# Kernel tuning notes

Measured on AMD Instinct MI355X. Metric: run time of the kernel, lower is better.

The kernel has to match this reference:

```python
import jax, jax.numpy as jnp
import numpy as np

N_NODES = 100000
N_EDGES = 1600000
F_IN = 64
HEADS = 4
F_OUT = 16
NEG_SLOPE = 0.2


def setup_inputs() -> dict:
    key = jax.random.key(0)
    k1, k2, k3, k4, k5 = jax.random.split(key, 5)
    x = jax.random.normal(k1, (N_NODES, F_IN), dtype=jnp.float32)
    edge_index = jax.random.randint(k2, (2, N_EDGES), 0, N_NODES, dtype=jnp.int64)
    # Glorot-ish scaled params
    W = jax.random.normal(k3, (HEADS, F_IN, F_OUT), dtype=jnp.float32) / np.sqrt(F_IN)
    a_src = jax.random.normal(k4, (HEADS, F_OUT), dtype=jnp.float32) / np.sqrt(F_OUT)
    a_dst = jax.random.normal(k5, (HEADS, F_OUT), dtype=jnp.float32) / np.sqrt(F_OUT)
    bias = jnp.zeros((HEADS * F_OUT,), dtype=jnp.float32)
    return {"x": x, "edge_index": edge_index, "W": W, "a_src": a_src,
            "a_dst": a_dst, "bias": bias}


def reference(x, edge_index, W, a_src, a_dst, bias):
    """Graph-attention conv (GAT-style) over a point-cloud graph.

    x: [N, F_in] node features; edge_index: [2, E] (src, dst);
    W: [H, F_in, F_out]; a_src/a_dst: [H, F_out]; bias: [H*F_out].
    Returns [N, H*F_out].
    """
    N = x.shape[0]
    src, dst = edge_index[0], edge_index[1]

    # Per-head linear projection: [N, H, F_out]
    h = jnp.einsum('nf,hfo->nho', x, W)

    # Per-node attention logits (decomposed GAT form): [N, H]
    logit_s = jnp.einsum('nho,ho->nh', h, a_src)
    logit_d = jnp.einsum('nho,ho->nh', h, a_dst)

    # Per-edge raw attention: [E, H]
    e = jax.nn.leaky_relu(logit_s[src] + logit_d[dst], negative_slope=NEG_SLOPE)

    # Segment softmax over incoming edges of each dst node
    m = jax.ops.segment_max(e, dst, num_segments=N)        # [N, H]
    m = jax.lax.stop_gradient(m)                           # softmax shift invariance
    e_exp = jnp.exp(e - m[dst])                            # [E, H]
    denom = jax.ops.segment_sum(e_exp, dst, num_segments=N)  # [N, H]
    alpha = e_exp / (denom[dst] + 1e-16)                   # [E, H]

    # Weighted message aggregation: scatter-add to dst
    msg = h[src] * alpha[:, :, None]                       # [E, H, F_out]
    out = jax.ops.segment_sum(msg, dst, num_segments=N)    # [N, H, F_out]

    return out.reshape(N, -1) + bias
```

## Files before the change

### kernel.cpp

```cpp
#include <hip/hip_runtime.h>

constexpr int N_NODES_C = 100000;
constexpr int N_EDGES_C = 1600000;
constexpr int F_IN_C = 64;
constexpr int HEADS_C = 4;
constexpr int F_OUT_C = 16;
constexpr float NEG_SLOPE_C = 0.2f;

constexpr int BUCK_SHIFT = 8;
constexpr int BUCK_NODES = 1 << BUCK_SHIFT;
constexpr int NBUCK = (N_NODES_C + BUCK_NODES - 1) / BUCK_NODES;
constexpr int BUCK_CAP = 5120;
constexpr int PART_BLOCKS = 256;
constexpr int EDGES_PER_PART_BLOCK = (N_EDGES_C + PART_BLOCKS - 1) / PART_BLOCKS;

typedef __attribute__((ext_vector_type(8))) short short8v;
typedef __attribute__((ext_vector_type(4))) float f32x4;

static __device__ __forceinline__ unsigned short f2bf(float f)
{
    const unsigned u = __float_as_uint(f);
    return (unsigned short)((u + 0x7FFF + ((u >> 16) & 1)) >> 16);
}
static __device__ __forceinline__ float bf2f(unsigned short b)
{
    return __uint_as_float(((unsigned)b) << 16);
}

__global__ __launch_bounds__(256) void k_prep(
    const float* __restrict__ W, int* __restrict__ bucket_cursor,
    unsigned short* __restrict__ Bpack)
{
    const int t = threadIdx.x;
    for (int i = t; i < NBUCK; i += 256) bucket_cursor[i] = 0;
    for (int idx = t; idx < 4096; idx += 256) {
        const int j    = idx & 7;
        const int lane = (idx >> 3) & 63;
        const int nt   = (idx >> 9) & 3;
        const int kc   = (idx >> 11) & 1;
        const int col  = nt * 16 + (lane & 15);
        const int k    = kc * 32 + (lane >> 4) * 8 + j;
        Bpack[idx] = f2bf(W[(col >> 4) * 1024 + k * 16 + (col & 15)]);
    }
}

__global__ __launch_bounds__(256) void k_project(
    const float* __restrict__ x, const unsigned short* __restrict__ Bpack,
    const float* __restrict__ a_src, const float* __restrict__ a_dst,
    unsigned short* __restrict__ h, float* __restrict__ ls, float* __restrict__ ld)
{
    const int wid  = threadIdx.x >> 6;
    const int lane = threadIdx.x & 63;
    const int node0 = (blockIdx.x * 4 + wid) * 16;
    const int colg = lane & 15;
    const int kg   = lane >> 4;

    const int rowc = min(node0 + colg, N_NODES_C - 1);
    short8v afrag[2];
    #pragma unroll
    for (int kc = 0; kc < 2; ++kc) {
        const float4* xp = (const float4*)&x[(size_t)rowc * 64 + kc * 32 + kg * 8];
        const float4 q0 = xp[0];
        const float4 q1 = xp[1];
        afrag[kc][0] = (short)f2bf(q0.x); afrag[kc][1] = (short)f2bf(q0.y);
        afrag[kc][2] = (short)f2bf(q0.z); afrag[kc][3] = (short)f2bf(q0.w);
        afrag[kc][4] = (short)f2bf(q1.x); afrag[kc][5] = (short)f2bf(q1.y);
        afrag[kc][6] = (short)f2bf(q1.z); afrag[kc][7] = (short)f2bf(q1.w);
    }

    f32x4 acc[4] = {{0.f,0.f,0.f,0.f},{0.f,0.f,0.f,0.f},
                    {0.f,0.f,0.f,0.f},{0.f,0.f,0.f,0.f}};
    #pragma unroll
    for (int kc = 0; kc < 2; ++kc) {
        #pragma unroll
        for (int nt = 0; nt < 4; ++nt) {
            const short8v bfrag = *(const short8v*)&Bpack[((kc * 4 + nt) * 64 + lane) * 8];
            acc[nt] = __builtin_amdgcn_mfma_f32_16x16x32_bf16(afrag[kc], bfrag, acc[nt], 0, 0, 0);
        }
    }

    #pragma unroll
    for (int nt = 0; nt < 4; ++nt) {
        const float as_v = a_src[nt * 16 + colg];
        const float ad_v = a_dst[nt * 16 + colg];
        #pragma unroll
        for (int i = 0; i < 4; ++i) {
            const int node = node0 + kg * 4 + i;
            const float hv = acc[nt][i];
            float vs = hv * as_v;
            float vd = hv * ad_v;
            #pragma unroll
            for (int o = 8; o >= 1; o >>= 1) {
                vs += __shfl_xor(vs, o, 64);
                vd += __shfl_xor(vd, o, 64);
            }
            if (node < N_NODES_C) {
                h[(size_t)node * 64 + nt * 16 + colg] = f2bf(hv);
                if (colg == 0) {
                    ls[node * HEADS_C + nt] = vs;
                    ld[node * HEADS_C + nt] = vd;
                }
            }
        }
    }
}

__global__ __launch_bounds__(1024) void k_partition(
    const int* __restrict__ src, const int* __restrict__ dst,
    int* __restrict__ bucket_cursor, int* __restrict__ bucketed)
{
    __shared__ int cnt[NBUCK];
    __shared__ int base[NBUCK];
    const int t = threadIdx.x;
    for (int i = t; i < NBUCK; i += 1024) cnt[i] = 0;
    __syncthreads();
    const int e0 = blockIdx.x * EDGES_PER_PART_BLOCK;
    const int e1 = min(e0 + EDGES_PER_PART_BLOCK, N_EDGES_C);
    for (int e = e0 + t; e < e1; e += 1024)
        atomicAdd(&cnt[dst[e] >> BUCK_SHIFT], 1);
    __syncthreads();
    for (int i = t; i < NBUCK; i += 1024) {
        base[i] = atomicAdd(&bucket_cursor[i], cnt[i]);
        cnt[i] = 0;
    }
    __syncthreads();
    for (int e = e0 + t; e < e1; e += 1024) {
        const int d = dst[e];
        const int b = d >> BUCK_SHIFT;
        const int r = atomicAdd(&cnt[b], 1);
        const int p = base[b] + r;
        if (p < BUCK_CAP)
            bucketed[b * BUCK_CAP + p] = src[e] | ((d & (BUCK_NODES - 1)) << 17);
    }
}

__global__ __launch_bounds__(256) void k_buildcsr(
    const int* __restrict__ bucket_cursor, const int* __restrict__ bucketed,
    int* __restrict__ csr_src, int* __restrict__ off, int* __restrict__ deg)
{
    __shared__ int hist[BUCK_NODES];
    __shared__ int pfx[BUCK_NODES];
    __shared__ int stageIn[BUCK_CAP];
    __shared__ int stageOut[BUCK_CAP];
    const int b = blockIdx.x;
    const int t = threadIdx.x;
    const int node0 = b * BUCK_NODES;
    const int nNodes = min(BUCK_NODES, N_NODES_C - node0);
    const int cnt = min(bucket_cursor[b], BUCK_CAP);
    const int* eb = &bucketed[(size_t)b * BUCK_CAP];

    hist[t] = 0;
    __syncthreads();
    for (int e = t; e < cnt; e += 256) {
        const int v = eb[e];
        stageIn[e] = v;
        atomicAdd(&hist[v >> 17], 1);
    }
    __syncthreads();
    const int myDeg = hist[t];
    pfx[t] = myDeg;
    __syncthreads();
    #pragma unroll
    for (int o = 1; o < BUCK_NODES; o <<= 1) {
        const int v = (t >= o) ? pfx[t - o] : 0;
        __syncthreads();
        pfx[t] += v;
        __syncthreads();
    }
    const int excl = pfx[t] - myDeg;
    if (t < nNodes) {
        deg[node0 + t] = myDeg;
        off[node0 + t] = b * BUCK_CAP + excl;
    }
    pfx[t] = excl;
    __syncthreads();
    for (int e = t; e < cnt; e += 256) {
        const int v = stageIn[e];
        const int r = atomicAdd(&pfx[v >> 17], 1);
        stageOut[r] = v & 0x1FFFF;
    }
    __syncthreads();
    int* outp = &csr_src[(size_t)b * BUCK_CAP];
    for (int e = t; e < cnt; e += 256) outp[e] = stageOut[e];
}

__global__ __launch_bounds__(256) void k_aggregate(
    const int* __restrict__ csr_src, const int* __restrict__ off,
    const int* __restrict__ deg, const float* __restrict__ ls,
    const float* __restrict__ ld, const unsigned short* __restrict__ h,
    const float* __restrict__ bias, float* __restrict__ out)
{
    const int wid  = threadIdx.x >> 6;
    const int lane = threadIdx.x & 63;
    const int d = blockIdx.x * 4 + wid;
    if (d >= N_NODES_C) return;
    const int hd = lane >> 4;
    const int jj = lane & 15;
    const int pb = (lane & 48) << 2;

    const int start = off[d];
    const int dg    = deg[d];
    const float ldv = ld[d * HEADS_C + hd];

    float acc  = 0.f;
    float denp = 0.f;

    for (int base = 0; base < dg; base += 16) {
        const int nIn = min(16, dg - base);
        int s_l = 0;
        float p_l = 0.f;
        if (jj < nIn) {
            s_l = csr_src[start + base + jj];
            float v = ls[s_l * HEADS_C + hd] + ldv;
            v = (v > 0.f) ? v : v * NEG_SLOPE_C;
            p_l = __expf(v);
        }
        denp += p_l;

        unsigned short hv[16];
        #pragma unroll
        for (int j = 0; j < 16; ++j) {
            const int s_j = __builtin_amdgcn_readlane(s_l, j);
            hv[j] = h[(size_t)(unsigned)s_j * 64 + lane];
        }
        #pragma unroll
        for (int j = 0; j < 16; ++j) {
            const int   pi  = __builtin_amdgcn_ds_bpermute(pb + (j << 2),
                                                           __float_as_int(p_l));
            const float p_j = __int_as_float(pi);
            acc = fmaf(p_j, bf2f(hv[j]), acc);
        }
    }
    #pragma unroll
    for (int o = 8; o >= 1; o >>= 1) denp += __shfl_xor(denp, o, 64);
    out[(size_t)d * 64 + lane] = acc / (denp + 1e-16f) + bias[lane];
}

extern "C" void kernel_launch(void* const* d_in, const int* in_sizes, int n_in,
                              void* d_out, int out_size, void* d_ws, size_t ws_size,
                              hipStream_t stream)
{
    const float* x     = (const float*)d_in[0];
    const int*   ei    = (const int*)d_in[1];
    const float* W     = (const float*)d_in[2];
    const float* a_src = (const float*)d_in[3];
    const float* a_dst = (const float*)d_in[4];
    const float* bias  = (const float*)d_in[5];
    float* out = (float*)d_out;

    float* ws   = (float*)d_ws;
    unsigned short* h = (unsigned short*)ws;
    float* ls   = (float*)(h + (size_t)N_NODES_C * 64);
    float* ld   = ls + (size_t)N_NODES_C * HEADS_C;
    int* bucket_cursor = (int*)(ld + (size_t)N_NODES_C * HEADS_C);
    int* deg     = bucket_cursor + NBUCK;
    int* off     = deg + N_NODES_C;
    int* bucketed = off + N_NODES_C;
    int* csr_src  = bucketed + (size_t)NBUCK * BUCK_CAP;
    unsigned short* Bpack = (unsigned short*)(csr_src + (size_t)NBUCK * BUCK_CAP);

    const int* src = ei;
    const int* dst = ei + N_EDGES_C;

    k_prep<<<1, 256, 0, stream>>>(W, bucket_cursor, Bpack);
    k_project<<<(N_NODES_C + 63) / 64, 256, 0, stream>>>(x, Bpack, a_src, a_dst, h, ls, ld);
    k_partition<<<PART_BLOCKS, 1024, 0, stream>>>(src, dst, bucket_cursor, bucketed);
    k_buildcsr<<<NBUCK, 256, 0, stream>>>(bucket_cursor, bucketed, csr_src, off, deg);
    k_aggregate<<<(N_NODES_C + 3) / 4, 256, 0, stream>>>(csr_src, off, deg, ls, ld, h, bias, out);
}
```

Measured before the change: 106.3 us.

## Fold attention vectors into projection MFMA, stage partition edges in LDS, unroll aggregation

Three changes. First, k_prep precomputes W·a_src and W·a_dst as an extra bf16 B fragment, so k_project gets the per-node logits from one more MFMA instead of shuffle reductions. Second, k_partition caches the packed edge and its bucket in LDS, so src/dst are read from global memory only once. Third, k_aggregate handles nodes of degree 16 or less in a single pass and processes higher-degree nodes in chunks of 32 edges, exposing more gather loads in flight. The costs are bf16 rounding of the folded logit weights, much more LDS in the 1024-thread partition block, and higher register use in the aggregation kernel.

```diff
diff --git a/kernel.cpp b/kernel.cpp
--- a/kernel.cpp
+++ b/kernel.cpp
@@ -28,11 +28,18 @@
 }
 
 __global__ __launch_bounds__(256) void k_prep(
-    const float* __restrict__ W, int* __restrict__ bucket_cursor,
-    unsigned short* __restrict__ Bpack)
-{
+    const float* __restrict__ W, const float* __restrict__ a_src,
+    const float* __restrict__ a_dst, int* __restrict__ bucket_cursor,
+    unsigned short* __restrict__ Bpack, unsigned short* __restrict__ Bpack2)
+{
+    __shared__ float sW[HEADS_C * F_IN_C * F_OUT_C];
+    __shared__ float sA[2 * HEADS_C * F_OUT_C];
     const int t = threadIdx.x;
     for (int i = t; i < NBUCK; i += 256) bucket_cursor[i] = 0;
+    for (int i = t; i < HEADS_C * F_IN_C * F_OUT_C; i += 256) sW[i] = W[i];
+    if (t < HEADS_C * F_OUT_C) { sA[t] = a_src[t]; sA[64 + t] = a_dst[t]; }
+    __syncthreads();
+
     for (int idx = t; idx < 4096; idx += 256) {
         const int j    = idx & 7;
         const int lane = (idx >> 3) & 63;
@@ -40,13 +47,29 @@
         const int kc   = (idx >> 11) & 1;
         const int col  = nt * 16 + (lane & 15);
         const int k    = kc * 32 + (lane >> 4) * 8 + j;
-        Bpack[idx] = f2bf(W[(col >> 4) * 1024 + k * 16 + (col & 15)]);
+        Bpack[idx] = f2bf(sW[(col >> 4) * 1024 + k * 16 + (col & 15)]);
+    }
+    for (int idx = t; idx < 1024; idx += 256) {
+        const int j    = idx & 7;
+        const int lane = (idx >> 3) & 63;
+        const int kc   = (idx >> 9) & 1;
+        const int col  = lane & 15;
+        const int k    = kc * 32 + (lane >> 4) * 8 + j;
+        float v = 0.f;
+        if (col < 8) {
+            const int hd = col & 3;
+            const float* wrow = &sW[hd * 1024 + k * 16];
+            const float* av   = &sA[(col < 4 ? 0 : 64) + hd * 16];
+            #pragma unroll
+            for (int o = 0; o < 16; ++o) v = fmaf(wrow[o], av[o], v);
+        }
+        Bpack2[idx] = f2bf(v);
     }
 }
 
 __global__ __launch_bounds__(256) void k_project(
     const float* __restrict__ x, const unsigned short* __restrict__ Bpack,
-    const float* __restrict__ a_src, const float* __restrict__ a_dst,
+    const unsigned short* __restrict__ Bpack2,
     unsigned short* __restrict__ h, float* __restrict__ ls, float* __restrict__ ld)
 {
     const int wid  = threadIdx.x >> 6;
@@ -70,6 +93,7 @@
 
     f32x4 acc[4] = {{0.f,0.f,0.f,0.f},{0.f,0.f,0.f,0.f},
                     {0.f,0.f,0.f,0.f},{0.f,0.f,0.f,0.f}};
+    f32x4 accL = {0.f,0.f,0.f,0.f};
     #pragma unroll
     for (int kc = 0; kc < 2; ++kc) {
         #pragma unroll
@@ -77,30 +101,25 @@
             const short8v bfrag = *(const short8v*)&Bpack[((kc * 4 + nt) * 64 + lane) * 8];
             acc[nt] = __builtin_amdgcn_mfma_f32_16x16x32_bf16(afrag[kc], bfrag, acc[nt], 0, 0, 0);
         }
+        const short8v bfrag2 = *(const short8v*)&Bpack2[(kc * 64 + lane) * 8];
+        accL = __builtin_amdgcn_mfma_f32_16x16x32_bf16(afrag[kc], bfrag2, accL, 0, 0, 0);
     }
 
     #pragma unroll
     for (int nt = 0; nt < 4; ++nt) {
-        const float as_v = a_src[nt * 16 + colg];
-        const float ad_v = a_dst[nt * 16 + colg];
         #pragma unroll
         for (int i = 0; i < 4; ++i) {
             const int node = node0 + kg * 4 + i;
-            const float hv = acc[nt][i];
-            float vs = hv * as_v;
-            float vd = hv * ad_v;
-            #pragma unroll
-            for (int o = 8; o >= 1; o >>= 1) {
-                vs += __shfl_xor(vs, o, 64);
-                vd += __shfl_xor(vd, o, 64);
-            }
-            if (node < N_NODES_C) {
-                h[(size_t)node * 64 + nt * 16 + colg] = f2bf(hv);
-                if (colg == 0) {
-                    ls[node * HEADS_C + nt] = vs;
-                    ld[node * HEADS_C + nt] = vd;
-                }
-            }
+            if (node < N_NODES_C)
+                h[(size_t)node * 64 + nt * 16 + colg] = f2bf(acc[nt][i]);
+        }
+    }
+    #pragma unroll
+    for (int i = 0; i < 4; ++i) {
+        const int node = node0 + kg * 4 + i;
+        if (node < N_NODES_C) {
+            if (colg < 4)      ls[node * HEADS_C + colg]       = accL[i];
+            else if (colg < 8) ld[node * HEADS_C + (colg - 4)] = accL[i];
         }
     }
 }
@@ -111,26 +130,32 @@
 {
     __shared__ int cnt[NBUCK];
     __shared__ int base[NBUCK];
+    __shared__ unsigned spack[EDGES_PER_PART_BLOCK];
+    __shared__ unsigned short sbuck[EDGES_PER_PART_BLOCK];
     const int t = threadIdx.x;
     for (int i = t; i < NBUCK; i += 1024) cnt[i] = 0;
     __syncthreads();
     const int e0 = blockIdx.x * EDGES_PER_PART_BLOCK;
-    const int e1 = min(e0 + EDGES_PER_PART_BLOCK, N_EDGES_C);
-    for (int e = e0 + t; e < e1; e += 1024)
-        atomicAdd(&cnt[dst[e] >> BUCK_SHIFT], 1);
+    const int nE = min(EDGES_PER_PART_BLOCK, N_EDGES_C - e0);
+    for (int e = t; e < nE; e += 1024) {
+        const int d = dst[e0 + e];
+        const int b = d >> BUCK_SHIFT;
+        spack[e] = (unsigned)src[e0 + e] | ((unsigned)(d & (BUCK_NODES - 1)) << 17);
+        sbuck[e] = (unsigned short)b;
+        atomicAdd(&cnt[b], 1);
+    }
     __syncthreads();
     for (int i = t; i < NBUCK; i += 1024) {
         base[i] = atomicAdd(&bucket_cursor[i], cnt[i]);
         cnt[i] = 0;
     }
     __syncthreads();
-    for (int e = e0 + t; e < e1; e += 1024) {
-        const int d = dst[e];
-        const int b = d >> BUCK_SHIFT;
+    for (int e = t; e < nE; e += 1024) {
+        const int b = sbuck[e];
         const int r = atomicAdd(&cnt[b], 1);
         const int p = base[b] + r;
         if (p < BUCK_CAP)
-            bucketed[b * BUCK_CAP + p] = src[e] | ((d & (BUCK_NODES - 1)) << 17);
+            bucketed[b * BUCK_CAP + p] = (int)spack[e];
     }
 }
 
@@ -205,18 +230,15 @@
     float acc  = 0.f;
     float denp = 0.f;
 
-    for (int base = 0; base < dg; base += 16) {
-        const int nIn = min(16, dg - base);
-        int s_l = 0;
-        float p_l = 0.f;
-        if (jj < nIn) {
-            s_l = csr_src[start + base + jj];
+    if (dg <= 16) {
+        int s_l = 0; float p_l = 0.f;
+        if (jj < dg) {
+            s_l = csr_src[start + jj];
             float v = ls[s_l * HEADS_C + hd] + ldv;
             v = (v > 0.f) ? v : v * NEG_SLOPE_C;
             p_l = __expf(v);
         }
-        denp += p_l;
-
+        denp = p_l;
         unsigned short hv[16];
         #pragma unroll
         for (int j = 0; j < 16; ++j) {
@@ -225,10 +247,43 @@
         }
         #pragma unroll
         for (int j = 0; j < 16; ++j) {
-            const int   pi  = __builtin_amdgcn_ds_bpermute(pb + (j << 2),
-                                                           __float_as_int(p_l));
-            const float p_j = __int_as_float(pi);
-            acc = fmaf(p_j, bf2f(hv[j]), acc);
+            const int pi = __builtin_amdgcn_ds_bpermute(pb + (j << 2), __float_as_int(p_l));
+            acc = fmaf(__int_as_float(pi), bf2f(hv[j]), acc);
+        }
+    } else {
+        for (int base = 0; base < dg; base += 32) {
+            const int rem  = dg - base;
+            const int nIn0 = min(16, rem);
+            const int nIn1 = min(16, max(0, rem - 16));
+            int s0 = 0, s1 = 0; float p0 = 0.f, p1 = 0.f;
+            if (jj < nIn0) {
+                s0 = csr_src[start + base + jj];
+                float v = ls[s0 * HEADS_C + hd] + ldv;
+                v = (v > 0.f) ? v : v * NEG_SLOPE_C;
+                p0 = __expf(v);
+            }
+            if (jj < nIn1) {
+                s1 = csr_src[start + base + 16 + jj];
+                float v = ls[s1 * HEADS_C + hd] + ldv;
+                v = (v > 0.f) ? v : v * NEG_SLOPE_C;
+                p1 = __expf(v);
+            }
+            denp += p0 + p1;
+            unsigned short hv0[16], hv1[16];
+            #pragma unroll
+            for (int j = 0; j < 16; ++j) {
+                const int sj0 = __builtin_amdgcn_readlane(s0, j);
+                hv0[j] = h[(size_t)(unsigned)sj0 * 64 + lane];
+                const int sj1 = __builtin_amdgcn_readlane(s1, j);
+                hv1[j] = h[(size_t)(unsigned)sj1 * 64 + lane];
+            }
+            #pragma unroll
+            for (int j = 0; j < 16; ++j) {
+                const int pi0 = __builtin_amdgcn_ds_bpermute(pb + (j << 2), __float_as_int(p0));
+                acc = fmaf(__int_as_float(pi0), bf2f(hv0[j]), acc);
+                const int pi1 = __builtin_amdgcn_ds_bpermute(pb + (j << 2), __float_as_int(p1));
+                acc = fmaf(__int_as_float(pi1), bf2f(hv1[j]), acc);
+            }
         }
     }
     #pragma unroll
@@ -257,13 +312,14 @@
     int* off     = deg + N_NODES_C;
     int* bucketed = off + N_NODES_C;
     int* csr_src  = bucketed + (size_t)NBUCK * BUCK_CAP;
-    unsigned short* Bpack = (unsigned short*)(csr_src + (size_t)NBUCK * BUCK_CAP);
+    unsigned short* Bpack  = (unsigned short*)(csr_src + (size_t)NBUCK * BUCK_CAP);
+    unsigned short* Bpack2 = Bpack + 4096;
 
     const int* src = ei;
     const int* dst = ei + N_EDGES_C;
 
-    k_prep<<<1, 256, 0, stream>>>(W, bucket_cursor, Bpack);
-    k_project<<<(N_NODES_C + 63) / 64, 256, 0, stream>>>(x, Bpack, a_src, a_dst, h, ls, ld);
+    k_prep<<<1, 256, 0, stream>>>(W, a_src, a_dst, bucket_cursor, Bpack, Bpack2);
+    k_project<<<(N_NODES_C + 63) / 64, 256, 0, stream>>>(x, Bpack, Bpack2, h, ls, ld);
     k_partition<<<PART_BLOCKS, 1024, 0, stream>>>(src, dst, bucket_cursor, bucketed);
     k_buildcsr<<<NBUCK, 256, 0, stream>>>(bucket_cursor, bucketed, csr_src, off, deg);
     k_aggregate<<<(N_NODES_C + 3) / 4, 256, 0, stream>>>(csr_src, off, deg, ls, ld, h, bias, out);
```

New measurement: 100.0 us. 5.9% less time.
